# Performance work log

Hardware: AMD Instinct MI355X
Metric: run time of the kernel (lower is better)

The kernel has to match this reference:

```python
import jax, jax.numpy as jnp
import numpy as np

EMB = 1536   # emb_dim
RANK = 32
N3 = 204     # modules with in_dim=3840 (6 per layer x 34 layers)
N10 = 34     # modules with in_dim=10240 (1 per layer x 34 layers)


def setup_inputs() -> dict:
    key = jax.random.key(0)
    ks = jax.random.split(key, 9)
    s = lambda k, shp: jax.random.normal(k, shp, dtype=jnp.float32)
    return {
        "x": s(ks[0], (EMB,)),
        "Wp3": s(ks[1], (N3, RANK * RANK, EMB)) * 0.02,   # stacked proj.weight for d=3840 group
        "bp3": s(ks[2], (N3, RANK * RANK)) * 0.02,        # stacked proj.bias
        "Wp10": s(ks[3], (N10, RANK * RANK, EMB)) * 0.02,
        "bp10": s(ks[4], (N10, RANK * RANK)) * 0.02,
        "A3": s(ks[5], (N3, RANK, 3840)),                 # stacked lora_a (rank, in_dim)
        "A10": s(ks[6], (N10, RANK, 10240)),
        "B3": s(ks[7], (N3, 3840, RANK)),                 # stacked lora_b (out_dim, rank); out_dim=3840 group
        "B10": s(ks[8], (N10, 10240, RANK)),
    }


def reference(x, Wp3, bp3, Wp10, bp10, A3, A10, B3, B10):
    # Batched version of the per-module torch loop:
    #   P = proj(x).view(rank, rank);  lora_a_out = P @ lora_a;  lora_b_out = lora_b
    # proj is a GEMV per module -> batched as one einsum per in_dim group.
    P3 = (jnp.einsum('nke,e->nk', Wp3, x) + bp3).reshape(N3, RANK, RANK)    # [N3,32,32]
    P10 = (jnp.einsum('nke,e->nk', Wp10, x) + bp10).reshape(N10, RANK, RANK)  # [N10,32,32]
    la3 = jnp.einsum('nij,njd->nid', P3, A3)      # [N3,32,3840]
    la10 = jnp.einsum('nij,njd->nid', P10, A10)   # [N10,32,10240]
    # lora_b weights are returned unchanged (pass-through), as in the torch module.
    return (la3, la10, B3, B10)
```

## Files before the change

### kernel.cpp

```cpp
#include <hip/hip_runtime.h>

#define EMB   1536
#define RANK  32
#define RANK2 1024
#define N3    204
#define N10   34
#define D3    3840
#define D10   10240

#define ROWS3  (N3 * RANK2)
#define ROWS10 (N10 * RANK2)

#define BPM3   (D3 / 256)
#define BPM10  (D10 / 256)
#define PA3_BLOCKS  (N3 * BPM3)
#define PA10_BLOCKS (N10 * BPM10)

#define SZ_LA3  ((size_t)N3  * RANK * D3)
#define SZ_LA10 ((size_t)N10 * RANK * D10)

#define CP_F4_PER_BLOCK 4096
#define CP3_BLOCKS  ((int)(SZ_LA3  / 4 / CP_F4_PER_BLOCK))
#define CP10_BLOCKS ((int)(SZ_LA10 / 4 / CP_F4_PER_BLOCK))

__global__ void gemv_all(const float* __restrict__ W3,
                         const float* __restrict__ b3,
                         const float* __restrict__ W10,
                         const float* __restrict__ b10,
                         const float* __restrict__ x,
                         float* __restrict__ P3,
                         float* __restrict__ P10) {
    const int wave = blockIdx.x * (blockDim.x >> 6) + (threadIdx.x >> 6);
    const int lane = threadIdx.x & 63;

    const float* W;
    const float* b;
    float* P;
    int row;
    if (wave < ROWS3) {
        W = W3; b = b3; P = P3; row = wave;
    } else {
        W = W10; b = b10; P = P10; row = wave - ROWS3;
    }

    const float* w = W + (size_t)row * EMB;
    float acc = 0.f;
#pragma unroll
    for (int it = 0; it < EMB / 256; ++it) {
        const int e = (it * 64 + lane) * 4;
        const float4 wv = *reinterpret_cast<const float4*>(w + e);
        const float4 xv = *reinterpret_cast<const float4*>(x + e);
        acc = fmaf(wv.x, xv.x, acc);
        acc = fmaf(wv.y, xv.y, acc);
        acc = fmaf(wv.z, xv.z, acc);
        acc = fmaf(wv.w, xv.w, acc);
    }
#pragma unroll
    for (int off = 32; off > 0; off >>= 1)
        acc += __shfl_down(acc, off);
    if (lane == 0) P[row] = acc + b[row];
}

__device__ __forceinline__ void pa_block(const float* __restrict__ P,
                                         const float* __restrict__ A,
                                         float* __restrict__ out,
                                         int module, int dblk, int D) {
    __shared__ float Ps[RANK2];
    for (int i = threadIdx.x; i < RANK2; i += blockDim.x)
        Ps[i] = P[(size_t)module * RANK2 + i];
    __syncthreads();

    const int d = dblk * blockDim.x + threadIdx.x;
    const float* a = A + (size_t)module * RANK * D + d;
    float av[RANK];
#pragma unroll
    for (int j = 0; j < RANK; ++j)
        av[j] = a[(size_t)j * D];

    float* o = out + (size_t)module * RANK * D + d;
#pragma unroll
    for (int i = 0; i < RANK; ++i) {
        float acc = 0.f;
#pragma unroll
        for (int j = 0; j < RANK; ++j)
            acc = fmaf(Ps[i * RANK + j], av[j], acc);
        o[(size_t)i * D] = acc;
    }
}

__device__ __forceinline__ void copy_block(const float4* __restrict__ src,
                                           float4* __restrict__ dst,
                                           int chunk) {
    const size_t base = (size_t)chunk * CP_F4_PER_BLOCK + threadIdx.x;
#pragma unroll
    for (int it = 0; it < CP_F4_PER_BLOCK / 256; ++it)
        dst[base + it * 256] = src[base + it * 256];
}

__global__ void fused_b(const float* __restrict__ P3,
                        const float* __restrict__ A3,
                        float* __restrict__ la3,
                        const float* __restrict__ P10,
                        const float* __restrict__ A10,
                        float* __restrict__ la10,
                        const float4* __restrict__ B3,
                        float4* __restrict__ oB3,
                        const float4* __restrict__ B10,
                        float4* __restrict__ oB10) {
    int bid = blockIdx.x;
    if (bid < PA3_BLOCKS) {
        pa_block(P3, A3, la3, bid / BPM3, bid % BPM3, D3);
        return;
    }
    bid -= PA3_BLOCKS;
    if (bid < PA10_BLOCKS) {
        pa_block(P10, A10, la10, bid / BPM10, bid % BPM10, D10);
        return;
    }
    bid -= PA10_BLOCKS;
    if (bid < CP3_BLOCKS) {
        copy_block(B3, oB3, bid);
        return;
    }
    bid -= CP3_BLOCKS;
    copy_block(B10, oB10, bid);
}

extern "C" void kernel_launch(void* const* d_in, const int* in_sizes, int n_in,
                              void* d_out, int out_size, void* d_ws, size_t ws_size,
                              hipStream_t stream) {
    const float* x    = (const float*)d_in[0];
    const float* Wp3  = (const float*)d_in[1];
    const float* bp3  = (const float*)d_in[2];
    const float* Wp10 = (const float*)d_in[3];
    const float* bp10 = (const float*)d_in[4];
    const float* A3   = (const float*)d_in[5];
    const float* A10  = (const float*)d_in[6];
    const float* B3   = (const float*)d_in[7];
    const float* B10  = (const float*)d_in[8];

    float* out = (float*)d_out;

    float* P3  = (float*)d_ws;
    float* P10 = P3 + (size_t)N3 * RANK2;

    float* la3  = out;
    float* la10 = out + SZ_LA3;
    float* oB3  = la10 + SZ_LA10;
    float* oB10 = oB3 + SZ_LA3;

    gemv_all<<<(ROWS3 + ROWS10) / 4, 256, 0, stream>>>(
        Wp3, bp3, Wp10, bp10, x, P3, P10);

    const int total_blocks = PA3_BLOCKS + PA10_BLOCKS + CP3_BLOCKS + CP10_BLOCKS;
    fused_b<<<total_blocks, 256, 0, stream>>>(
        P3, A3, la3, P10, A10, la10,
        (const float4*)B3, (float4*)oB3,
        (const float4*)B10, (float4*)oB10);
}
```

Measured before the change: 367.6 us.

## Move B pass-through copy into GEMV kernel and vectorize P@A with float4

The lora_b pass-through copy now runs in the first kernel alongside the projection GEMV, since the copy does not depend on P. The second kernel does only the P@A product. Each thread there handles four columns with float4 loads and stores, and P rows are read from shared memory as float4. The aim is to overlap the independent copy with the GEMV and to cut per-element instruction overhead in the P@A stage, at the cost of higher register pressure (128 floats of A per thread).

```diff
diff --git a/kernel.cpp b/kernel.cpp
--- a/kernel.cpp
+++ b/kernel.cpp
@@ -10,83 +10,19 @@
 
 #define ROWS3  (N3 * RANK2)
 #define ROWS10 (N10 * RANK2)
-
-#define BPM3   (D3 / 256)
-#define BPM10  (D10 / 256)
-#define PA3_BLOCKS  (N3 * BPM3)
-#define PA10_BLOCKS (N10 * BPM10)
+#define GEMV_BLOCKS ((ROWS3 + ROWS10) / 4)
 
 #define SZ_LA3  ((size_t)N3  * RANK * D3)
 #define SZ_LA10 ((size_t)N10 * RANK * D10)
 
 #define CP_F4_PER_BLOCK 4096
-#define CP3_BLOCKS  ((int)(SZ_LA3  / 4 / CP_F4_PER_BLOCK))
-#define CP10_BLOCKS ((int)(SZ_LA10 / 4 / CP_F4_PER_BLOCK))
+#define CP3_BLOCKS  1530
+#define CP10_BLOCKS 680
 
-__global__ void gemv_all(const float* __restrict__ W3,
-                         const float* __restrict__ b3,
-                         const float* __restrict__ W10,
-                         const float* __restrict__ b10,
-                         const float* __restrict__ x,
-                         float* __restrict__ P3,
-                         float* __restrict__ P10) {
-    const int wave = blockIdx.x * (blockDim.x >> 6) + (threadIdx.x >> 6);
-    const int lane = threadIdx.x & 63;
-
-    const float* W;
-    const float* b;
-    float* P;
-    int row;
-    if (wave < ROWS3) {
-        W = W3; b = b3; P = P3; row = wave;
-    } else {
-        W = W10; b = b10; P = P10; row = wave - ROWS3;
-    }
-
-    const float* w = W + (size_t)row * EMB;
-    float acc = 0.f;
-#pragma unroll
-    for (int it = 0; it < EMB / 256; ++it) {
-        const int e = (it * 64 + lane) * 4;
-        const float4 wv = *reinterpret_cast<const float4*>(w + e);
-        const float4 xv = *reinterpret_cast<const float4*>(x + e);
-        acc = fmaf(wv.x, xv.x, acc);
-        acc = fmaf(wv.y, xv.y, acc);
-        acc = fmaf(wv.z, xv.z, acc);
-        acc = fmaf(wv.w, xv.w, acc);
-    }
-#pragma unroll
-    for (int off = 32; off > 0; off >>= 1)
-        acc += __shfl_down(acc, off);
-    if (lane == 0) P[row] = acc + b[row];
-}
-
-__device__ __forceinline__ void pa_block(const float* __restrict__ P,
-                                         const float* __restrict__ A,
-                                         float* __restrict__ out,
-                                         int module, int dblk, int D) {
-    __shared__ float Ps[RANK2];
-    for (int i = threadIdx.x; i < RANK2; i += blockDim.x)
-        Ps[i] = P[(size_t)module * RANK2 + i];
-    __syncthreads();
-
-    const int d = dblk * blockDim.x + threadIdx.x;
-    const float* a = A + (size_t)module * RANK * D + d;
-    float av[RANK];
-#pragma unroll
-    for (int j = 0; j < RANK; ++j)
-        av[j] = a[(size_t)j * D];
-
-    float* o = out + (size_t)module * RANK * D + d;
-#pragma unroll
-    for (int i = 0; i < RANK; ++i) {
-        float acc = 0.f;
-#pragma unroll
-        for (int j = 0; j < RANK; ++j)
-            acc = fmaf(Ps[i * RANK + j], av[j], acc);
-        o[(size_t)i * D] = acc;
-    }
-}
+#define PA3_CHUNKS  4
+#define PA10_CHUNKS 10
+#define PA3_BLOCKS  (N3 * PA3_CHUNKS)
+#define PA10_BLOCKS (N10 * PA10_CHUNKS)
 
 __device__ __forceinline__ void copy_block(const float4* __restrict__ src,
                                            float4* __restrict__ dst,
@@ -97,33 +33,113 @@
         dst[base + it * 256] = src[base + it * 256];
 }
 
-__global__ void fused_b(const float* __restrict__ P3,
-                        const float* __restrict__ A3,
-                        float* __restrict__ la3,
-                        const float* __restrict__ P10,
-                        const float* __restrict__ A10,
-                        float* __restrict__ la10,
-                        const float4* __restrict__ B3,
-                        float4* __restrict__ oB3,
-                        const float4* __restrict__ B10,
-                        float4* __restrict__ oB10) {
+__global__ void k1_gemv_copy(const float* __restrict__ W3,
+                             const float* __restrict__ b3,
+                             const float* __restrict__ W10,
+                             const float* __restrict__ b10,
+                             const float* __restrict__ x,
+                             float* __restrict__ P3,
+                             float* __restrict__ P10,
+                             const float4* __restrict__ B3,
+                             float4* __restrict__ oB3,
+                             const float4* __restrict__ B10,
+                             float4* __restrict__ oB10) {
     int bid = blockIdx.x;
-    if (bid < PA3_BLOCKS) {
-        pa_block(P3, A3, la3, bid / BPM3, bid % BPM3, D3);
+    if (bid < GEMV_BLOCKS) {
+        const int wave = bid * 4 + (threadIdx.x >> 6);
+        const int lane = threadIdx.x & 63;
+
+        const float* W;
+        const float* b;
+        float* P;
+        int row;
+        if (wave < ROWS3) {
+            W = W3; b = b3; P = P3; row = wave;
+        } else {
+            W = W10; b = b10; P = P10; row = wave - ROWS3;
+        }
+
+        const float* w = W + (size_t)row * EMB;
+        float acc = 0.f;
+#pragma unroll
+        for (int it = 0; it < EMB / 256; ++it) {
+            const int e = (it * 64 + lane) * 4;
+            const float4 wv = *reinterpret_cast<const float4*>(w + e);
+            const float4 xv = *reinterpret_cast<const float4*>(x + e);
+            acc = fmaf(wv.x, xv.x, acc);
+            acc = fmaf(wv.y, xv.y, acc);
+            acc = fmaf(wv.z, xv.z, acc);
+            acc = fmaf(wv.w, xv.w, acc);
+        }
+#pragma unroll
+        for (int off = 32; off > 0; off >>= 1)
+            acc += __shfl_down(acc, off);
+        if (lane == 0) P[row] = acc + b[row];
         return;
     }
-    bid -= PA3_BLOCKS;
-    if (bid < PA10_BLOCKS) {
-        pa_block(P10, A10, la10, bid / BPM10, bid % BPM10, D10);
-        return;
+    bid -= GEMV_BLOCKS;
+    if (bid < CP3_BLOCKS) { copy_block(B3, oB3, bid); return; }
+    copy_block(B10, oB10, bid - CP3_BLOCKS);
+}
+
+__global__ __launch_bounds__(256) void k2_pa(const float* __restrict__ P3,
+                                             const float* __restrict__ A3,
+                                             float* __restrict__ la3,
+                                             const float* __restrict__ P10,
+                                             const float* __restrict__ A10,
+                                             float* __restrict__ la10) {
+    int bid = blockIdx.x;
+    const float* P; const float* A; float* la; int D, m, chunk;
+    if (bid < PA3_BLOCKS) {
+        m = bid >> 2; chunk = bid & 3;
+        P = P3; A = A3; la = la3; D = D3;
+    } else {
+        bid -= PA3_BLOCKS;
+        m = bid / PA10_CHUNKS; chunk = bid % PA10_CHUNKS;
+        P = P10; A = A10; la = la10; D = D10;
     }
-    bid -= PA10_BLOCKS;
-    if (bid < CP3_BLOCKS) {
-        copy_block(B3, oB3, bid);
-        return;
+
+    __shared__ float Ps[RANK2];
+    const float4* Pm4 = reinterpret_cast<const float4*>(P + (size_t)m * RANK2);
+    reinterpret_cast<float4*>(Ps)[threadIdx.x] = Pm4[threadIdx.x];
+    __syncthreads();
+
+    const int d0 = chunk * 1024 + (int)threadIdx.x * 4;
+    if (d0 >= D) return;
+
+    const float* a = A + (size_t)m * RANK * D + d0;
+    float4 av[RANK];
+#pragma unroll
+    for (int j = 0; j < RANK; ++j)
+        av[j] = *reinterpret_cast<const float4*>(a + (size_t)j * D);
+
+    const float4* Ps4 = reinterpret_cast<const float4*>(Ps);
+    float* o = la + (size_t)m * RANK * D + d0;
+#pragma unroll
+    for (int i = 0; i < RANK; ++i) {
+        float4 pr[8];
+#pragma unroll
+        for (int j8 = 0; j8 < 8; ++j8)
+            pr[j8] = Ps4[i * 8 + j8];
+        float4 acc = make_float4(0.f, 0.f, 0.f, 0.f);
+#pragma unroll
+        for (int j8 = 0; j8 < 8; ++j8) {
+            const float4 p4 = pr[j8];
+            const float4 a0 = av[j8 * 4 + 0];
+            const float4 a1 = av[j8 * 4 + 1];
+            const float4 a2 = av[j8 * 4 + 2];
+            const float4 a3 = av[j8 * 4 + 3];
+            acc.x = fmaf(p4.x, a0.x, acc.x); acc.y = fmaf(p4.x, a0.y, acc.y);
+            acc.z = fmaf(p4.x, a0.z, acc.z); acc.w = fmaf(p4.x, a0.w, acc.w);
+            acc.x = fmaf(p4.y, a1.x, acc.x); acc.y = fmaf(p4.y, a1.y, acc.y);
+            acc.z = fmaf(p4.y, a1.z, acc.z); acc.w = fmaf(p4.y, a1.w, acc.w);
+            acc.x = fmaf(p4.z, a2.x, acc.x); acc.y = fmaf(p4.z, a2.y, acc.y);
+            acc.z = fmaf(p4.z, a2.z, acc.z); acc.w = fmaf(p4.z, a2.w, acc.w);
+            acc.x = fmaf(p4.w, a3.x, acc.x); acc.y = fmaf(p4.w, a3.y, acc.y);
+            acc.z = fmaf(p4.w, a3.z, acc.z); acc.w = fmaf(p4.w, a3.w, acc.w);
+        }
+        *reinterpret_cast<float4*>(o + (size_t)i * D) = acc;
     }
-    bid -= CP3_BLOCKS;
-    copy_block(B10, oB10, bid);
 }
 
 extern "C" void kernel_launch(void* const* d_in, const int* in_sizes, int n_in,
@@ -149,12 +165,12 @@
     float* oB3  = la10 + SZ_LA10;
     float* oB10 = oB3 + SZ_LA3;
 
-    gemv_all<<<(ROWS3 + ROWS10) / 4, 256, 0, stream>>>(
-        Wp3, bp3, Wp10, bp10, x, P3, P10);
-
-    const int total_blocks = PA3_BLOCKS + PA10_BLOCKS + CP3_BLOCKS + CP10_BLOCKS;
-    fused_b<<<total_blocks, 256, 0, stream>>>(
-        P3, A3, la3, P10, A10, la10,
+    const int k1_blocks = GEMV_BLOCKS + CP3_BLOCKS + CP10_BLOCKS;
+    k1_gemv_copy<<<k1_blocks, 256, 0, stream>>>(
+        Wp3, bp3, Wp10, bp10, x, P3, P10,
         (const float4*)B3, (float4*)oB3,
         (const float4*)B10, (float4*)oB10);
+
+    k2_pa<<<PA3_BLOCKS + PA10_BLOCKS, 256, 0, stream>>>(
+        P3, A3, la3, P10, A10, la10);
 }
```

New measurement: 375.7 us. +2.2%, slower.
